# Optimization experiments

Measured on AMD Instinct MI355X. Metric: run time of the kernel, lower is better.

Reference implementation:

```python
import jax, jax.numpy as jnp
import numpy as np

DIM = 768
HEADS = 12
HID = 3072  # mlp_ratio * dim
BATCH = 8
FRAMES = 16
GRID = 14
NTOK = GRID * GRID
LN_EPS = 1e-5
EPS = 1e-6


def setup_inputs() -> dict:
    key = jax.random.key(0)
    ks = jax.random.split(key, 8)
    w = lambda k, shape: jax.random.normal(k, shape, jnp.float32) * 0.02
    return {
        "x": jax.random.normal(ks[0], (BATCH * FRAMES, NTOK, DIM), jnp.float32),
        "ln1_w": jnp.ones((DIM,), jnp.float32),
        "ln1_b": jnp.zeros((DIM,), jnp.float32),
        "qkv_w": w(ks[1], (3 * DIM, DIM)),
        "proj_w": w(ks[2], (DIM, DIM)),
        "proj_b": jnp.zeros((DIM,), jnp.float32),
        "ln2_w": jnp.ones((DIM,), jnp.float32),
        "ln2_b": jnp.zeros((DIM,), jnp.float32),
        "fc1_w": w(ks[3], (HID, DIM)),
        "fc1_b": jnp.zeros((HID,), jnp.float32),
        "dw_w": w(ks[4], (HID, 1, 3, 3)),
        "dw_b": jnp.zeros((HID,), jnp.float32),
        "fc2_w": w(ks[5], (DIM, HID)),
        "fc2_b": jnp.zeros((DIM,), jnp.float32),
        "H": GRID,
        "W": GRID,
        "num_frames": FRAMES,
    }


def _layernorm(x, w, b):
    mu = jnp.mean(x, axis=-1, keepdims=True)
    var = jnp.mean(jnp.square(x - mu), axis=-1, keepdims=True)
    return (x - mu) * jax.lax.rsqrt(var + LN_EPS) * w + b


def _joint_ts_attention(xn, qkv_w, proj_w, proj_b, num_frames):
    # xn: (b*f, n, c)
    Bt, n, C = xn.shape
    h = HEADS
    e = C // h
    scale = e ** (-0.5)
    qkv = jnp.einsum('bnc,dc->bnd', xn, qkv_w).reshape(Bt, n, 3, h, e)
    q, k, v = qkv[:, :, 0], qkv[:, :, 1], qkv[:, :, 2]
    # ReLU feature map + scale offset
    q_ = jax.nn.relu(q) + scale
    k_ = jax.nn.relu(k) + scale
    b = Bt // num_frames
    m = num_frames * n  # joint time-space sequence length
    q_ = q_.reshape(b, m, h, e)
    k_ = k_.reshape(b, m, h, e)
    v_ = v.reshape(b, m, h, e)
    # kv_: (b, h, e, e)
    kv = jnp.einsum('bnhe,bnhd->bhed', k_, v_)
    k_sum = jnp.sum(k_, axis=1)  # (b, h, e)
    z = 1.0 / (jnp.einsum('bnhe,bhe->bnh', q_, k_sum) + EPS)  # (b, m, h)
    out = jnp.einsum('bnhe,bhed->bnhd', q_, kv) * z[..., None]  # (b, m, h, e)
    out = out.reshape(Bt, n, C)
    return jnp.einsum('bnc,dc->bnd', out, proj_w) + proj_b


def _dwconv(x, w, b, H, W):
    # x: (B, N, C) -> NCHW depthwise 3x3, pad 1
    Bn, n, c = x.shape
    xi = jnp.transpose(x, (0, 2, 1)).reshape(Bn, c, H, W)
    y = jax.lax.conv_general_dilated(
        xi, w, window_strides=(1, 1), padding=((1, 1), (1, 1)),
        dimension_numbers=('NCHW', 'OIHW', 'NCHW'), feature_group_count=c)
    y = y + b[None, :, None, None]
    return jnp.transpose(y.reshape(Bn, c, n), (0, 2, 1))


def reference(x, ln1_w, ln1_b, qkv_w, proj_w, proj_b, ln2_w, ln2_b,
              fc1_w, fc1_b, dw_w, dw_b, fc2_w, fc2_b, H, W, num_frames):
    # x = x + attn(norm1(x), num_frames)
    x = x + _joint_ts_attention(_layernorm(x, ln1_w, ln1_b), qkv_w, proj_w, proj_b, num_frames)
    # x = x + mlp(norm2(x), H, W)
    xn = _layernorm(x, ln2_w, ln2_b)
    hdn = jnp.einsum('bnc,hc->bnh', xn, fc1_w) + fc1_b
    hdn = _dwconv(hdn, dw_w, dw_b, H, W)
    hdn = jax.nn.gelu(hdn, approximate=False)
    out = jnp.einsum('bnh,ch->bnc', hdn, fc2_w) + fc2_b
    return x + out
```

## Files before the change

kernel.cpp:

```cpp
#include <hip/hip_runtime.h>

typedef unsigned short u16;
typedef unsigned int u32;

typedef __bf16 bf16x8 __attribute__((ext_vector_type(8)));
typedef float f32x4 __attribute__((ext_vector_type(4)));

#define DIM 768
#define HID 3072
#define NTOK 196
#define BT 128
#define NTOKENS (BT * NTOK)
#define MJ 3136
#define HEADS 12

#define QB_ELE ((size_t)NTOKENS * 768)

#define SZ_WB   ((size_t)(2304*768 + 768*768 + 3072*768 + 768*3072) * 2)
#define SZ_XN   ((size_t)NTOKENS * DIM * 2)
#define SZ_QKV  ((size_t)NTOKENS * 2304 * 2)
#define SZ_X2   ((size_t)NTOKENS * DIM * 4)
#define SZ_HDN  ((size_t)NTOKENS * HID * 2)
#define SZ_KV   ((size_t)96 * 4096 * 4)
#define SZ_KS   ((size_t)96 * 64 * 4)
#define WS_NEED (SZ_WB + SZ_XN + SZ_QKV + SZ_X2 + SZ_HDN + SZ_KV + SZ_KS)

static void* g_buf = nullptr;

__device__ __forceinline__ float b2f(u16 u) {
  union { u32 i; float f; } x; x.i = ((u32)u) << 16; return x.f;
}
__device__ __forceinline__ u16 f2b(float f) {
  u32 x = __float_as_uint(f);
  return (u16)((x + 0x7fffu + ((x >> 16) & 1u)) >> 16);
}

__device__ __forceinline__ void gload_lds16(const u16* g, u16* l) {
  __builtin_amdgcn_global_load_lds(
      (const __attribute__((address_space(1))) u32*)g,
      (__attribute__((address_space(3))) u32*)l, 16, 0, 0);
}

#define N4_QKV   442368
#define N4_PROJ  147456
#define N4_FC1   589824
#define N4_FC2   589824
#define N4_ALL   (N4_QKV + N4_PROJ + N4_FC1 + N4_FC2)
__global__ __launch_bounds__(256) void cvt_all(const float* __restrict__ a,
    const float* __restrict__ b, const float* __restrict__ c,
    const float* __restrict__ d, u16* __restrict__ out)
{
  int i = blockIdx.x * 256 + threadIdx.x;
  if (i >= N4_ALL) return;
  const float* src;
  int j = i;
  if (j < N4_QKV) { src = a; }
  else if ((j -= N4_QKV) < N4_PROJ) { src = b; }
  else if ((j -= N4_PROJ) < N4_FC1) { src = c; }
  else { j -= N4_FC1; src = d; }
  float4 f = ((const float4*)src)[j];
  ushort4 r;
  r.x = f2b(f.x); r.y = f2b(f.y); r.z = f2b(f.z); r.w = f2b(f.w);
  ((ushort4*)out)[i] = r;
}

__global__ __launch_bounds__(256) void zero_f32(float* __restrict__ p, int n) {
  int i = blockIdx.x * 256 + threadIdx.x;
  if (i < n) p[i] = 0.0f;
}

__global__ __launch_bounds__(256) void ln_kernel(const float* __restrict__ xin,
    const float* __restrict__ w, const float* __restrict__ b, u16* __restrict__ out)
{
  const int token = blockIdx.x * 4 + (threadIdx.x >> 6);
  const int lane = threadIdx.x & 63;
  float v[12];
  const float* x = xin + (size_t)token * DIM;
#pragma unroll
  for (int c = 0; c < 3; ++c) {
    float4 f = *(const float4*)(x + c * 256 + lane * 4);
    v[c*4+0] = f.x; v[c*4+1] = f.y; v[c*4+2] = f.z; v[c*4+3] = f.w;
  }
  float s = 0.f, sq = 0.f;
#pragma unroll
  for (int i = 0; i < 12; ++i) { s += v[i]; sq += v[i] * v[i]; }
#pragma unroll
  for (int off = 32; off > 0; off >>= 1) {
    s += __shfl_xor(s, off, 64);
    sq += __shfl_xor(sq, off, 64);
  }
  const float mean = s * (1.0f / 768.0f);
  const float var = sq * (1.0f / 768.0f) - mean * mean;
  const float rstd = rsqrtf(var + 1e-5f);
  u16* o = out + (size_t)token * DIM;
#pragma unroll
  for (int c = 0; c < 3; ++c) {
    float4 wv = *(const float4*)(w + c * 256 + lane * 4);
    float4 bv = *(const float4*)(b + c * 256 + lane * 4);
    ushort4 r;
    r.x = f2b((v[c*4+0] - mean) * rstd * wv.x + bv.x);
    r.y = f2b((v[c*4+1] - mean) * rstd * wv.y + bv.y);
    r.z = f2b((v[c*4+2] - mean) * rstd * wv.z + bv.z);
    r.w = f2b((v[c*4+3] - mean) * rstd * wv.w + bv.w);
    *(ushort4*)(o + c * 256 + lane * 4) = r;
  }
}

template<int MODE, int NF, int NXT, int NN, int KK>
__global__ __launch_bounds__(512, 2) void gemm8(
    const u16* __restrict__ A, const u16* __restrict__ W,
    const float* __restrict__ bias, const float* __restrict__ res,
    void* __restrict__ out)
{
  extern __shared__ char smem[];
  u16* As = (u16*)smem;
  u16* Bs = (u16*)(smem + 65536);

  const int t = threadIdx.x;
  const int l = t & 63;
  const int w = t >> 6;
  const int wm = w >> 2;
  const int wn = w & 3;
  constexpr int NR = NF - 2;

  constexpr int TOTAL = 98 * NXT;
  constexpr int Q8 = TOTAL >> 3;
  constexpr int R8 = TOTAL & 7;
  const int orig = blockIdx.x;
  const int xcd = orig & 7;
  const int idx = orig >> 3;
  const int wg = (xcd < R8) ? (xcd * (Q8 + 1) + idx)
                            : (R8 * (Q8 + 1) + (xcd - R8) * Q8 + idx);
  const int m0 = (wg / NXT) * 256;
  const int n0 = (wg % NXT) * (NF * 64);

  const int scol = ((l & 7) ^ (l >> 3)) * 8;
  const u16* gA = A + (size_t)(m0 + w * 8 + (l >> 3)) * KK + scol;
  const u16* gB = W + (size_t)(n0 + w * 8 + (l >> 3)) * KK + scol;
  u16* lA = As + w * 512;
  u16* lB = Bs + w * 512;

#define STAGE_A(bb, u, kt) \
    gload_lds16(gA + (size_t)(u) * 64 * KK + (size_t)(kt) * 64, \
                lA + (bb) * 16384 + (u) * 4096)
#define STAGE_B(bb, u, kt) \
    gload_lds16(gB + (size_t)(u) * 64 * KK + (size_t)(kt) * 64, \
                lB + (bb) * NF * 4096 + (u) * 4096)

  const int lm = l & 15;
  const int qq = l >> 4;
  const int acol = (qq << 4) ^ ((l & 7) << 4);
  const int abase = (wm * 128 + lm) * 128 + acol;
  const int bbase = (wn * (NF * 16) + lm) * 128 + acol;

  f32x4 acc[8][NF];
#pragma unroll
  for (int mi = 0; mi < 8; ++mi)
#pragma unroll
    for (int ni = 0; ni < NF; ++ni) acc[mi][ni] = (f32x4){0.f, 0.f, 0.f, 0.f};

  constexpr int NT = KK / 64;

#pragma unroll
  for (int u = 0; u < 4; ++u) STAGE_A(0, u, 0);
#pragma unroll
  for (int u = 0; u < NF; ++u) STAGE_B(0, u, 0);
#pragma unroll
  for (int u = 0; u < 4; ++u) STAGE_A(1, u, 1);
  asm volatile("s_waitcnt vmcnt(4)" ::: "memory");
  __builtin_amdgcn_s_barrier();

  for (int ti = 0; ti < NT; ++ti) {
    const int cb = ti & 1, nb = cb ^ 1;
    const char* Ac = (const char*)As + cb * 32768;
    const char* Bc = (const char*)Bs + cb * (NF * 8192);
    bf16x8 a0[4][2], a1[4][2], b01[2][2], bx[NR][2];

#pragma unroll
    for (int mi = 0; mi < 4; ++mi) {
      const int off = abase + mi * 2048;
      a0[mi][0] = *(const bf16x8*)(Ac + off);
      a0[mi][1] = *(const bf16x8*)(Ac + (off ^ 64));
    }
#pragma unroll
    for (int ni = 0; ni < 2; ++ni) {
      const int off = bbase + ni * 2048;
      b01[ni][0] = *(const bf16x8*)(Bc + off);
      b01[ni][1] = *(const bf16x8*)(Bc + (off ^ 64));
    }
    if (ti + 1 < NT) { STAGE_B(nb, 0, ti + 1); STAGE_B(nb, 1, ti + 1); }
    __builtin_amdgcn_s_setprio(1);
#pragma unroll
    for (int mi = 0; mi < 4; ++mi)
#pragma unroll
      for (int ni = 0; ni < 2; ++ni) {
        acc[mi][ni] = __builtin_amdgcn_mfma_f32_16x16x32_bf16(a0[mi][0], b01[ni][0], acc[mi][ni], 0, 0, 0);
        acc[mi][ni] = __builtin_amdgcn_mfma_f32_16x16x32_bf16(a0[mi][1], b01[ni][1], acc[mi][ni], 0, 0, 0);
      }
    __builtin_amdgcn_s_setprio(0);

#pragma unroll
    for (int ni = 0; ni < NR; ++ni) {
      const int off = bbase + (ni + 2) * 2048;
      bx[ni][0] = *(const bf16x8*)(Bc + off);
      bx[ni][1] = *(const bf16x8*)(Bc + (off ^ 64));
    }
    if (ti + 1 < NT) {
#pragma unroll
      for (int u = 2; u < NF; ++u) STAGE_B(nb, u, ti + 1);
    }
    __builtin_amdgcn_s_setprio(1);
#pragma unroll
    for (int mi = 0; mi < 4; ++mi)
#pragma unroll
      for (int ni = 0; ni < NR; ++ni) {
        acc[mi][ni + 2] = __builtin_amdgcn_mfma_f32_16x16x32_bf16(a0[mi][0], bx[ni][0], acc[mi][ni + 2], 0, 0, 0);
        acc[mi][ni + 2] = __builtin_amdgcn_mfma_f32_16x16x32_bf16(a0[mi][1], bx[ni][1], acc[mi][ni + 2], 0, 0, 0);
      }
    __builtin_amdgcn_s_setprio(0);

#pragma unroll
    for (int mi = 0; mi < 4; ++mi) {
      const int off = abase + 8192 + mi * 2048;
      a1[mi][0] = *(const bf16x8*)(Ac + off);
      a1[mi][1] = *(const bf16x8*)(Ac + (off ^ 64));
    }
    __builtin_amdgcn_s_setprio(1);
#pragma unroll
    for (int mi = 0; mi < 4; ++mi)
#pragma unroll
      for (int ni = 0; ni < NR; ++ni) {
        acc[mi + 4][ni + 2] = __builtin_amdgcn_mfma_f32_16x16x32_bf16(a1[mi][0], bx[ni][0], acc[mi + 4][ni + 2], 0, 0, 0);
        acc[mi + 4][ni + 2] = __builtin_amdgcn_mfma_f32_16x16x32_bf16(a1[mi][1], bx[ni][1], acc[mi + 4][ni + 2], 0, 0, 0);
      }
    __builtin_amdgcn_s_setprio(0);

    asm volatile("s_waitcnt lgkmcnt(0)" ::: "memory");
    __builtin_amdgcn_s_barrier();

    if (ti + 2 < NT) {
#pragma unroll
      for (int u = 0; u < 4; ++u) STAGE_A(cb, u, ti + 2);
    }

    __builtin_amdgcn_s_setprio(1);
#pragma unroll
    for (int mi = 0; mi < 4; ++mi)
#pragma unroll
      for (int ni = 0; ni < 2; ++ni) {
        acc[mi + 4][ni] = __builtin_amdgcn_mfma_f32_16x16x32_bf16(a1[mi][0], b01[ni][0], acc[mi + 4][ni], 0, 0, 0);
        acc[mi + 4][ni] = __builtin_amdgcn_mfma_f32_16x16x32_bf16(a1[mi][1], b01[ni][1], acc[mi + 4][ni], 0, 0, 0);
      }
    __builtin_amdgcn_s_setprio(0);

    if (ti + 2 < NT) {
      asm volatile("s_waitcnt vmcnt(4)" ::: "memory");
    } else {
      asm volatile("s_waitcnt vmcnt(0)" ::: "memory");
    }
    __builtin_amdgcn_s_barrier();
  }
#undef STAGE_A
#undef STAGE_B

#pragma unroll
  for (int mi = 0; mi < 8; ++mi) {
    const int rbase = m0 + wm * 128 + mi * 16 + qq * 4;
    const int b = rbase / 3136;
    const int mj = rbase - b * 3136;
#pragma unroll
    for (int ni = 0; ni < NF; ++ni) {
      const int col = n0 + wn * (NF * 16) + ni * 16 + lm;
      if (MODE == 0) {
        if (col < 768) {
#pragma unroll
          for (int r = 0; r < 4; ++r) {
            float v = fmaxf(acc[mi][ni][r], 0.0f) + 0.125f;
            ((u16*)out)[(size_t)(rbase + r) * 768 + col] = f2b(v);
          }
        } else {
          const bool isV = (col >= 1536);
          const int cc = col - (isV ? 1536 : 768);
          const int h = cc >> 6, e = cc & 63;
          ushort4 pk;
          float v0 = acc[mi][ni][0], v1 = acc[mi][ni][1];
          float v2 = acc[mi][ni][2], v3 = acc[mi][ni][3];
          if (!isV) {
            v0 = fmaxf(v0, 0.0f) + 0.125f; v1 = fmaxf(v1, 0.0f) + 0.125f;
            v2 = fmaxf(v2, 0.0f) + 0.125f; v3 = fmaxf(v3, 0.0f) + 0.125f;
          }
          pk.x = f2b(v0); pk.y = f2b(v1); pk.z = f2b(v2); pk.w = f2b(v3);
          u16* dst = (u16*)out + (isV ? 2 * QB_ELE : QB_ELE)
                   + ((size_t)((b * 12 + h) * 64 + e)) * 3136 + mj;
          *(ushort4*)dst = pk;
        }
      } else {
        const float bv = bias[col];
#pragma unroll
        for (int r = 0; r < 4; ++r) {
          float v = acc[mi][ni][r];
          const size_t idxo = (size_t)(rbase + r) * NN + col;
          if (MODE == 1) {
            ((float*)out)[idxo] = v + bv + res[idxo];
          } else if (MODE == 2) {
            ((u16*)out)[idxo] = f2b(v + bv);
          } else {
            ((float*)out)[idxo] = v + bv + res[idxo];
          }
        }
      }
    }
  }
}

__global__ __launch_bounds__(256) void ksum_kernel(const u16* __restrict__ KT,
    float* __restrict__ KS)
{
  const int bh = blockIdx.x;
  const int t = threadIdx.x;
  const int w = t >> 6, l = t & 63;
  const u16* base = KT + (size_t)(bh * 64 + w * 16) * 3136;
  for (int r = 0; r < 16; ++r) {
    float s = 0.f;
    const u16* row = base + (size_t)r * 3136;
#pragma unroll
    for (int p = 0; p < 7; ++p) {
      const int m = p * 512 + l * 8;
      if (m < 3136) {
        bf16x8 v = *(const bf16x8*)(row + m);
#pragma unroll
        for (int j = 0; j < 8; ++j) s += (float)v[j];
      }
    }
#pragma unroll
    for (int off = 32; off > 0; off >>= 1) s += __shfl_xor(s, off, 64);
    if (l == 0) KS[bh * 64 + w * 16 + r] = s;
  }
}

__global__ __launch_bounds__(256) void kv_mfma(const u16* __restrict__ KT,
    const u16* __restrict__ VT, float* __restrict__ kv)
{
  const int bh = blockIdx.x;
  const int s = blockIdx.y;
  const int t = threadIdx.x;
  const int l = t & 63, w = t >> 6;
  const int lm = l & 15, qq = l >> 4;
  const size_t mj0 = (size_t)s * 448;
  const u16* ka = KT + (size_t)(bh * 64 + w * 16 + lm) * 3136 + mj0 + qq * 8;
  const u16* vb = VT + (size_t)(bh * 64 + lm) * 3136 + mj0 + qq * 8;

  f32x4 acc[4];
#pragma unroll
  for (int ni = 0; ni < 4; ++ni) acc[ni] = (f32x4){0.f, 0.f, 0.f, 0.f};

#pragma unroll 4
  for (int kk = 0; kk < 14; ++kk) {
    bf16x8 a = *(const bf16x8*)(ka + kk * 32);
#pragma unroll
    for (int ni = 0; ni < 4; ++ni) {
      bf16x8 b = *(const bf16x8*)(vb + (size_t)ni * 16 * 3136 + kk * 32);
      acc[ni] = __builtin_amdgcn_mfma_f32_16x16x32_bf16(a, b, acc[ni], 0, 0, 0);
    }
  }
  float* dst = kv + (size_t)bh * 4096;
#pragma unroll
  for (int ni = 0; ni < 4; ++ni)
#pragma unroll
    for (int r = 0; r < 4; ++r)
      atomicAdd(&dst[(w * 16 + qq * 4 + r) * 64 + ni * 16 + lm], acc[ni][r]);
}

__global__ __launch_bounds__(256) void attn_out(const u16* __restrict__ qb,
    const float* __restrict__ kv, const float* __restrict__ ksum,
    u16* __restrict__ outp)
{
  const int chunk = blockIdx.x;
  const int h = blockIdx.y;
  const int b = blockIdx.z;
  __shared__ float kvs[4096];
  __shared__ float kss[64];
  __shared__ float qs[4096];
  const int t = threadIdx.x;
  const float* kvsrc = kv + (size_t)(b * 12 + h) * 4096;
  for (int i = t; i < 1024; i += 256)
    ((float4*)kvs)[i] = ((const float4*)kvsrc)[i];
  if (t < 64) kss[t] = ksum[(b * 12 + h) * 64 + t];
  __syncthreads();
  const int wv = t >> 6, lane = t & 63;
  float* qw = &qs[wv * 1024];
  const size_t tok0 = (size_t)b * MJ + chunk * 64 + wv * 16;
#pragma unroll
  for (int i = 0; i < 16; ++i) {
    float q = b2f(qb[(tok0 + i) * 768 + h * 64 + lane]);
    float pd = q * kss[lane];
#pragma unroll
    for (int off = 32; off > 0; off >>= 1) pd += __shfl_xor(pd, off, 64);
    qw[i * 64 + lane] = q * (1.0f / (pd + 1e-6f));
  }
  float o[16];
#pragma unroll
  for (int i = 0; i < 16; ++i) o[i] = 0.f;
  for (int e = 0; e < 64; ++e) {
    const float kvc = kvs[e * 64 + lane];
#pragma unroll
    for (int i = 0; i < 16; ++i) o[i] += qw[i * 64 + e] * kvc;
  }
#pragma unroll
  for (int i = 0; i < 16; ++i)
    outp[(tok0 + i) * 768 + h * 64 + lane] = f2b(o[i]);
}

__global__ __launch_bounds__(256) void dwconv_gelu(u16* __restrict__ hdn,
    const float* __restrict__ w, const float* __restrict__ bias)
{
  __shared__ u16 pl[196 * 136];
  const int cb = blockIdx.x;
  const int fr = blockIdx.y;
  const int t = threadIdx.x;
  const int c0 = cb * 128;
  u16* base = hdn + (size_t)fr * 196 * HID + c0;
#pragma unroll
  for (int i = 0; i < 13; ++i) {
    int idx = i * 256 + t;
    if (idx < 3136) {
      int p = idx >> 4, cq = idx & 15;
      *(uint4*)&pl[p * 136 + cq * 8] = *(const uint4*)(base + (size_t)p * HID + cq * 8);
    }
  }
  __syncthreads();
  const int pc = t & 31;
  const int pg = t >> 5;
  const int cc = pc * 4;
  float wr[36];
#pragma unroll
  for (int k = 0; k < 9; ++k)
#pragma unroll
    for (int u = 0; u < 4; ++u) wr[k * 4 + u] = w[(c0 + cc + u) * 9 + k];
  float bv[4];
#pragma unroll
  for (int u = 0; u < 4; ++u) bv[u] = bias[c0 + cc + u];

  for (int j = 0; j < 25; ++j) {
    const int p = pg + j * 8;
    if (p >= 196) break;
    const int py = p / 14, px = p % 14;
    float a0 = bv[0], a1 = bv[1], a2 = bv[2], a3 = bv[3];
#pragma unroll
    for (int ky = 0; ky < 3; ++ky) {
      int yy = py + ky - 1;
      if (yy < 0 || yy > 13) continue;
#pragma unroll
      for (int kx = 0; kx < 3; ++kx) {
        int xx = px + kx - 1;
        if (xx < 0 || xx > 13) continue;
        ushort4 tv = *(const ushort4*)&pl[(yy * 14 + xx) * 136 + cc];
        const float* wk = &wr[(ky * 3 + kx) * 4];
        a0 += wk[0] * b2f(tv.x);
        a1 += wk[1] * b2f(tv.y);
        a2 += wk[2] * b2f(tv.z);
        a3 += wk[3] * b2f(tv.w);
      }
    }
    ushort4 r;
    r.x = f2b(0.5f * a0 * (1.0f + erff(a0 * 0.70710678118654752f)));
    r.y = f2b(0.5f * a1 * (1.0f + erff(a1 * 0.70710678118654752f)));
    r.z = f2b(0.5f * a2 * (1.0f + erff(a2 * 0.70710678118654752f)));
    r.w = f2b(0.5f * a3 * (1.0f + erff(a3 * 0.70710678118654752f)));
    *(ushort4*)(base + (size_t)p * HID + cc) = r;
  }
}

static void set_gemm_attrs() {
  (void)hipFuncSetAttribute(reinterpret_cast<const void*>(&gemm8<0, 4, 9, 2304, 768>),
                            hipFuncAttributeMaxDynamicSharedMemorySize, 131072);
  (void)hipFuncSetAttribute(reinterpret_cast<const void*>(&gemm8<1, 3, 4, 768, 768>),
                            hipFuncAttributeMaxDynamicSharedMemorySize, 114688);
  (void)hipFuncSetAttribute(reinterpret_cast<const void*>(&gemm8<2, 4, 12, 3072, 768>),
                            hipFuncAttributeMaxDynamicSharedMemorySize, 131072);
  (void)hipFuncSetAttribute(reinterpret_cast<const void*>(&gemm8<3, 3, 4, 768, 3072>),
                            hipFuncAttributeMaxDynamicSharedMemorySize, 114688);
}
struct WsInit {
  WsInit() {
    (void)hipMalloc(&g_buf, WS_NEED);
    set_gemm_attrs();
  }
};
static WsInit g_wsinit;

extern "C" void kernel_launch(void* const* d_in, const int* in_sizes, int n_in,
                              void* d_out, int out_size, void* d_ws, size_t ws_size,
                              hipStream_t stream)
{
  (void)in_sizes; (void)n_in; (void)out_size;
  static bool attrs_once = [] { set_gemm_attrs(); return true; }();
  (void)attrs_once;

  const float* x     = (const float*)d_in[0];
  const float* ln1w  = (const float*)d_in[1];
  const float* ln1b  = (const float*)d_in[2];
  const float* qkvw  = (const float*)d_in[3];
  const float* projw = (const float*)d_in[4];
  const float* projb = (const float*)d_in[5];
  const float* ln2w  = (const float*)d_in[6];
  const float* ln2b  = (const float*)d_in[7];
  const float* fc1w  = (const float*)d_in[8];
  const float* fc1b  = (const float*)d_in[9];
  const float* dww   = (const float*)d_in[10];
  const float* dwb   = (const float*)d_in[11];
  const float* fc2w  = (const float*)d_in[12];
  const float* fc2b  = (const float*)d_in[13];

  char* p = (ws_size >= WS_NEED) ? (char*)d_ws : (char*)g_buf;
  u16* WQKV  = (u16*)p;   p += (size_t)2304 * 768 * 2;
  u16* WPROJ = (u16*)p;   p += (size_t)768 * 768 * 2;
  u16* WFC1  = (u16*)p;   p += (size_t)3072 * 768 * 2;
  u16* WFC2  = (u16*)p;   p += (size_t)768 * 3072 * 2;
  u16* XN    = (u16*)p;   p += SZ_XN;
  u16* QKV   = (u16*)p;   p += SZ_QKV;
  float* X2  = (float*)p; p += SZ_X2;
  u16* HDN   = (u16*)p;   p += SZ_HDN;
  float* KV  = (float*)p; p += SZ_KV;
  float* KS  = (float*)p; p += SZ_KS;

  u16* KT = QKV + QB_ELE;
  u16* VT = QKV + 2 * QB_ELE;

  cvt_all<<<(N4_ALL + 255) / 256, 256, 0, stream>>>(qkvw, projw, fc1w, fc2w, WQKV);

  const int nz = 96 * 4096;
  zero_f32<<<(nz + 255) / 256, 256, 0, stream>>>(KV, nz);
  ln_kernel<<<NTOKENS / 4, 256, 0, stream>>>(x, ln1w, ln1b, XN);
  gemm8<0, 4, 9, 2304, 768><<<98 * 9, 512, 131072, stream>>>(XN, WQKV, nullptr, nullptr, QKV);
  ksum_kernel<<<96, 256, 0, stream>>>(KT, KS);
  kv_mfma<<<dim3(96, 7), 256, 0, stream>>>(KT, VT, KV);
  attn_out<<<dim3(49, 12, 8), 256, 0, stream>>>(QKV, KV, KS, XN);
  gemm8<1, 3, 4, 768, 768><<<98 * 4, 512, 114688, stream>>>(XN, WPROJ, projb, x, X2);
  ln_kernel<<<NTOKENS / 4, 256, 0, stream>>>(X2, ln2w, ln2b, QKV);
  gemm8<2, 4, 12, 3072, 768><<<98 * 12, 512, 131072, stream>>>(QKV, WFC1, fc1b, nullptr, HDN);
  dwconv_gelu<<<dim3(24, 128), 256, 0, stream>>>(HDN, dww, dwb);
  gemm8<3, 3, 4, 768, 3072><<<98 * 4, 512, 114688, stream>>>(HDN, WFC2, fc2b, X2, (float*)d_out);
}
```

Baseline: 909.5 us.

## Shrink GEMM tiles to 128 rows with 4 waves and single-buffered static LDS

The GEMM kernel moves from 256-row tiles with 8 waves and double-buffered dynamic LDS (up to 128KB) to 128-row tiles with 4 waves and a single static LDS buffer. Each k-step now waits for all loads, reads fragments, barriers, then issues the next tile's global loads before running the MFMAs. The grid doubles, which should raise occupancy and smooth wave quantization across CUs. In exchange, per-tile reuse drops, the hand-interleaved load/MFMA schedule is gone, and global-to-LDS latency is hidden only by other resident workgroups.

```diff
diff --git a/kernel.cpp b/kernel.cpp
--- a/kernel.cpp
+++ b/kernel.cpp
@@ -107,23 +107,21 @@
 }
 
 template<int MODE, int NF, int NXT, int NN, int KK>
-__global__ __launch_bounds__(512, 2) void gemm8(
+__global__ __launch_bounds__(256, 2) void gemm8(
     const u16* __restrict__ A, const u16* __restrict__ W,
     const float* __restrict__ bias, const float* __restrict__ res,
     void* __restrict__ out)
 {
-  extern __shared__ char smem[];
-  u16* As = (u16*)smem;
-  u16* Bs = (u16*)(smem + 65536);
+  __shared__ __align__(16) u16 As[128 * 64];
+  __shared__ __align__(16) u16 Bs[NF * 64 * 64];
 
   const int t = threadIdx.x;
   const int l = t & 63;
   const int w = t >> 6;
-  const int wm = w >> 2;
-  const int wn = w & 3;
-  constexpr int NR = NF - 2;
-
-  constexpr int TOTAL = 98 * NXT;
+  const int wmh = w >> 1;
+  const int wnh = w & 1;
+
+  constexpr int TOTAL = 196 * NXT;
   constexpr int Q8 = TOTAL >> 3;
   constexpr int R8 = TOTAL & 7;
   const int orig = blockIdx.x;
@@ -131,151 +129,95 @@
   const int idx = orig >> 3;
   const int wg = (xcd < R8) ? (xcd * (Q8 + 1) + idx)
                             : (R8 * (Q8 + 1) + (xcd - R8) * Q8 + idx);
-  const int m0 = (wg / NXT) * 256;
+  const int m0 = (wg / NXT) * 128;
   const int n0 = (wg % NXT) * (NF * 64);
 
   const int scol = ((l & 7) ^ (l >> 3)) * 8;
-  const u16* gA = A + (size_t)(m0 + w * 8 + (l >> 3)) * KK + scol;
-  const u16* gB = W + (size_t)(n0 + w * 8 + (l >> 3)) * KK + scol;
-  u16* lA = As + w * 512;
-  u16* lB = Bs + w * 512;
-
-#define STAGE_A(bb, u, kt) \
+  const u16* gA = A + (size_t)(m0 + w * 16 + (l >> 3)) * KK + scol;
+  const u16* gB = W + (size_t)(n0 + w * 16 + (l >> 3)) * KK + scol;
+  u16* lA = As + w * 1024;
+  u16* lB = Bs + w * 1024;
+
+#define STAGE_A(u, kt) do { \
     gload_lds16(gA + (size_t)(u) * 64 * KK + (size_t)(kt) * 64, \
-                lA + (bb) * 16384 + (u) * 4096)
-#define STAGE_B(bb, u, kt) \
+                lA + (u) * 4096); \
+    gload_lds16(gA + (size_t)(u) * 64 * KK + (size_t)8 * KK + (size_t)(kt) * 64, \
+                lA + (u) * 4096 + 512); } while (0)
+#define STAGE_B(u, kt) do { \
     gload_lds16(gB + (size_t)(u) * 64 * KK + (size_t)(kt) * 64, \
-                lB + (bb) * NF * 4096 + (u) * 4096)
+                lB + (u) * 4096); \
+    gload_lds16(gB + (size_t)(u) * 64 * KK + (size_t)8 * KK + (size_t)(kt) * 64, \
+                lB + (u) * 4096 + 512); } while (0)
+#define STAGE_ALL(kt) do { \
+    STAGE_A(0, kt); STAGE_A(1, kt); \
+    _Pragma("unroll") \
+    for (int u_ = 0; u_ < NF; ++u_) STAGE_B(u_, kt); } while (0)
 
   const int lm = l & 15;
   const int qq = l >> 4;
   const int acol = (qq << 4) ^ ((l & 7) << 4);
-  const int abase = (wm * 128 + lm) * 128 + acol;
-  const int bbase = (wn * (NF * 16) + lm) * 128 + acol;
-
-  f32x4 acc[8][NF];
-#pragma unroll
-  for (int mi = 0; mi < 8; ++mi)
-#pragma unroll
-    for (int ni = 0; ni < NF; ++ni) acc[mi][ni] = (f32x4){0.f, 0.f, 0.f, 0.f};
+  const int abase = (wmh * 64 + lm) * 128 + acol;
+  const int bbase = (wnh * (NF * 32) + lm) * 128 + acol;
+
+  f32x4 acc[4][2 * NF];
+#pragma unroll
+  for (int mi = 0; mi < 4; ++mi)
+#pragma unroll
+    for (int nj = 0; nj < 2 * NF; ++nj) acc[mi][nj] = (f32x4){0.f, 0.f, 0.f, 0.f};
 
   constexpr int NT = KK / 64;
 
-#pragma unroll
-  for (int u = 0; u < 4; ++u) STAGE_A(0, u, 0);
-#pragma unroll
-  for (int u = 0; u < NF; ++u) STAGE_B(0, u, 0);
-#pragma unroll
-  for (int u = 0; u < 4; ++u) STAGE_A(1, u, 1);
-  asm volatile("s_waitcnt vmcnt(4)" ::: "memory");
-  __builtin_amdgcn_s_barrier();
+  STAGE_ALL(0);
 
   for (int ti = 0; ti < NT; ++ti) {
-    const int cb = ti & 1, nb = cb ^ 1;
-    const char* Ac = (const char*)As + cb * 32768;
-    const char* Bc = (const char*)Bs + cb * (NF * 8192);
-    bf16x8 a0[4][2], a1[4][2], b01[2][2], bx[NR][2];
-
+    asm volatile("s_waitcnt vmcnt(0)" ::: "memory");
+    __builtin_amdgcn_s_barrier();
+
+    bf16x8 af[4][2], bfv[2 * NF][2];
 #pragma unroll
     for (int mi = 0; mi < 4; ++mi) {
       const int off = abase + mi * 2048;
-      a0[mi][0] = *(const bf16x8*)(Ac + off);
-      a0[mi][1] = *(const bf16x8*)(Ac + (off ^ 64));
-    }
-#pragma unroll
-    for (int ni = 0; ni < 2; ++ni) {
-      const int off = bbase + ni * 2048;
-      b01[ni][0] = *(const bf16x8*)(Bc + off);
-      b01[ni][1] = *(const bf16x8*)(Bc + (off ^ 64));
-    }
-    if (ti + 1 < NT) { STAGE_B(nb, 0, ti + 1); STAGE_B(nb, 1, ti + 1); }
+      af[mi][0] = *(const bf16x8*)((const char*)As + off);
+      af[mi][1] = *(const bf16x8*)((const char*)As + (off ^ 64));
+    }
+#pragma unroll
+    for (int nj = 0; nj < 2 * NF; ++nj) {
+      const int off = bbase + nj * 2048;
+      bfv[nj][0] = *(const bf16x8*)((const char*)Bs + off);
+      bfv[nj][1] = *(const bf16x8*)((const char*)Bs + (off ^ 64));
+    }
+    asm volatile("s_waitcnt lgkmcnt(0)" ::: "memory");
+    __builtin_amdgcn_s_barrier();
+
+    if (ti + 1 < NT) STAGE_ALL(ti + 1);
+
     __builtin_amdgcn_s_setprio(1);
 #pragma unroll
     for (int mi = 0; mi < 4; ++mi)
 #pragma unroll
-      for (int ni = 0; ni < 2; ++ni) {
-        acc[mi][ni] = __builtin_amdgcn_mfma_f32_16x16x32_bf16(a0[mi][0], b01[ni][0], acc[mi][ni], 0, 0, 0);
-        acc[mi][ni] = __builtin_amdgcn_mfma_f32_16x16x32_bf16(a0[mi][1], b01[ni][1], acc[mi][ni], 0, 0, 0);
+      for (int nj = 0; nj < 2 * NF; ++nj) {
+        acc[mi][nj] = __builtin_amdgcn_mfma_f32_16x16x32_bf16(af[mi][0], bfv[nj][0], acc[mi][nj], 0, 0, 0);
+        acc[mi][nj] = __builtin_amdgcn_mfma_f32_16x16x32_bf16(af[mi][1], bfv[nj][1], acc[mi][nj], 0, 0, 0);
       }
     __builtin_amdgcn_s_setprio(0);
-
-#pragma unroll
-    for (int ni = 0; ni < NR; ++ni) {
-      const int off = bbase + (ni + 2) * 2048;
-      bx[ni][0] = *(const bf16x8*)(Bc + off);
-      bx[ni][1] = *(const bf16x8*)(Bc + (off ^ 64));
-    }
-    if (ti + 1 < NT) {
-#pragma unroll
-      for (int u = 2; u < NF; ++u) STAGE_B(nb, u, ti + 1);
-    }
-    __builtin_amdgcn_s_setprio(1);
-#pragma unroll
-    for (int mi = 0; mi < 4; ++mi)
-#pragma unroll
-      for (int ni = 0; ni < NR; ++ni) {
-        acc[mi][ni + 2] = __builtin_amdgcn_mfma_f32_16x16x32_bf16(a0[mi][0], bx[ni][0], acc[mi][ni + 2], 0, 0, 0);
-        acc[mi][ni + 2] = __builtin_amdgcn_mfma_f32_16x16x32_bf16(a0[mi][1], bx[ni][1], acc[mi][ni + 2], 0, 0, 0);
-      }
-    __builtin_amdgcn_s_setprio(0);
-
-#pragma unroll
-    for (int mi = 0; mi < 4; ++mi) {
-      const int off = abase + 8192 + mi * 2048;
-      a1[mi][0] = *(const bf16x8*)(Ac + off);
-      a1[mi][1] = *(const bf16x8*)(Ac + (off ^ 64));
-    }
-    __builtin_amdgcn_s_setprio(1);
-#pragma unroll
-    for (int mi = 0; mi < 4; ++mi)
-#pragma unroll
-      for (int ni = 0; ni < NR; ++ni) {
-        acc[mi + 4][ni + 2] = __builtin_amdgcn_mfma_f32_16x16x32_bf16(a1[mi][0], bx[ni][0], acc[mi + 4][ni + 2], 0, 0, 0);
-        acc[mi + 4][ni + 2] = __builtin_amdgcn_mfma_f32_16x16x32_bf16(a1[mi][1], bx[ni][1], acc[mi + 4][ni + 2], 0, 0, 0);
-      }
-    __builtin_amdgcn_s_setprio(0);
-
-    asm volatile("s_waitcnt lgkmcnt(0)" ::: "memory");
-    __builtin_amdgcn_s_barrier();
-
-    if (ti + 2 < NT) {
-#pragma unroll
-      for (int u = 0; u < 4; ++u) STAGE_A(cb, u, ti + 2);
-    }
-
-    __builtin_amdgcn_s_setprio(1);
-#pragma unroll
-    for (int mi = 0; mi < 4; ++mi)
-#pragma unroll
-      for (int ni = 0; ni < 2; ++ni) {
-        acc[mi + 4][ni] = __builtin_amdgcn_mfma_f32_16x16x32_bf16(a1[mi][0], b01[ni][0], acc[mi + 4][ni], 0, 0, 0);
-        acc[mi + 4][ni] = __builtin_amdgcn_mfma_f32_16x16x32_bf16(a1[mi][1], b01[ni][1], acc[mi + 4][ni], 0, 0, 0);
-      }
-    __builtin_amdgcn_s_setprio(0);
-
-    if (ti + 2 < NT) {
-      asm volatile("s_waitcnt vmcnt(4)" ::: "memory");
-    } else {
-      asm volatile("s_waitcnt vmcnt(0)" ::: "memory");
-    }
-    __builtin_amdgcn_s_barrier();
   }
 #undef STAGE_A
 #undef STAGE_B
-
-#pragma unroll
-  for (int mi = 0; mi < 8; ++mi) {
-    const int rbase = m0 + wm * 128 + mi * 16 + qq * 4;
+#undef STAGE_ALL
+
+#pragma unroll
+  for (int mi = 0; mi < 4; ++mi) {
+    const int rbase = m0 + wmh * 64 + mi * 16 + qq * 4;
     const int b = rbase / 3136;
     const int mj = rbase - b * 3136;
 #pragma unroll
-    for (int ni = 0; ni < NF; ++ni) {
-      const int col = n0 + wn * (NF * 16) + ni * 16 + lm;
+    for (int nj = 0; nj < 2 * NF; ++nj) {
+      const int col = n0 + wnh * (NF * 32) + nj * 16 + lm;
       if (MODE == 0) {
         if (col < 768) {
 #pragma unroll
           for (int r = 0; r < 4; ++r) {
-            float v = fmaxf(acc[mi][ni][r], 0.0f) + 0.125f;
+            float v = fmaxf(acc[mi][nj][r], 0.0f) + 0.125f;
             ((u16*)out)[(size_t)(rbase + r) * 768 + col] = f2b(v);
           }
         } else {
@@ -283,8 +225,8 @@
           const int cc = col - (isV ? 1536 : 768);
           const int h = cc >> 6, e = cc & 63;
           ushort4 pk;
-          float v0 = acc[mi][ni][0], v1 = acc[mi][ni][1];
-          float v2 = acc[mi][ni][2], v3 = acc[mi][ni][3];
+          float v0 = acc[mi][nj][0], v1 = acc[mi][nj][1];
+          float v2 = acc[mi][nj][2], v3 = acc[mi][nj][3];
           if (!isV) {
             v0 = fmaxf(v0, 0.0f) + 0.125f; v1 = fmaxf(v1, 0.0f) + 0.125f;
             v2 = fmaxf(v2, 0.0f) + 0.125f; v3 = fmaxf(v3, 0.0f) + 0.125f;
@@ -298,7 +240,7 @@
         const float bv = bias[col];
 #pragma unroll
         for (int r = 0; r < 4; ++r) {
-          float v = acc[mi][ni][r];
+          float v = acc[mi][nj][r];
           const size_t idxo = (size_t)(rbase + r) * NN + col;
           if (MODE == 1) {
             ((float*)out)[idxo] = v + bv + res[idxo];
@@ -471,21 +413,8 @@
   }
 }
 
-static void set_gemm_attrs() {
-  (void)hipFuncSetAttribute(reinterpret_cast<const void*>(&gemm8<0, 4, 9, 2304, 768>),
-                            hipFuncAttributeMaxDynamicSharedMemorySize, 131072);
-  (void)hipFuncSetAttribute(reinterpret_cast<const void*>(&gemm8<1, 3, 4, 768, 768>),
-                            hipFuncAttributeMaxDynamicSharedMemorySize, 114688);
-  (void)hipFuncSetAttribute(reinterpret_cast<const void*>(&gemm8<2, 4, 12, 3072, 768>),
-                            hipFuncAttributeMaxDynamicSharedMemorySize, 131072);
-  (void)hipFuncSetAttribute(reinterpret_cast<const void*>(&gemm8<3, 3, 4, 768, 3072>),
-                            hipFuncAttributeMaxDynamicSharedMemorySize, 114688);
-}
 struct WsInit {
-  WsInit() {
-    (void)hipMalloc(&g_buf, WS_NEED);
-    set_gemm_attrs();
-  }
+  WsInit() { (void)hipMalloc(&g_buf, WS_NEED); }
 };
 static WsInit g_wsinit;
 
@@ -494,8 +423,6 @@
                               hipStream_t stream)
 {
   (void)in_sizes; (void)n_in; (void)out_size;
-  static bool attrs_once = [] { set_gemm_attrs(); return true; }();
-  (void)attrs_once;
 
   const float* x     = (const float*)d_in[0];
   const float* ln1w  = (const float*)d_in[1];
@@ -532,13 +459,13 @@
   const int nz = 96 * 4096;
   zero_f32<<<(nz + 255) / 256, 256, 0, stream>>>(KV, nz);
   ln_kernel<<<NTOKENS / 4, 256, 0, stream>>>(x, ln1w, ln1b, XN);
-  gemm8<0, 4, 9, 2304, 768><<<98 * 9, 512, 131072, stream>>>(XN, WQKV, nullptr, nullptr, QKV);
+  gemm8<0, 4, 9, 2304, 768><<<196 * 9, 256, 0, stream>>>(XN, WQKV, nullptr, nullptr, QKV);
   ksum_kernel<<<96, 256, 0, stream>>>(KT, KS);
   kv_mfma<<<dim3(96, 7), 256, 0, stream>>>(KT, VT, KV);
   attn_out<<<dim3(49, 12, 8), 256, 0, stream>>>(QKV, KV, KS, XN);
-  gemm8<1, 3, 4, 768, 768><<<98 * 4, 512, 114688, stream>>>(XN, WPROJ, projb, x, X2);
+  gemm8<1, 3, 4, 768, 768><<<196 * 4, 256, 0, stream>>>(XN, WPROJ, projb, x, X2);
   ln_kernel<<<NTOKENS / 4, 256, 0, stream>>>(X2, ln2w, ln2b, QKV);
-  gemm8<2, 4, 12, 3072, 768><<<98 * 12, 512, 131072, stream>>>(QKV, WFC1, fc1b, nullptr, HDN);
+  gemm8<2, 4, 12, 3072, 768><<<196 * 12, 256, 0, stream>>>(QKV, WFC1, fc1b, nullptr, HDN);
   dwconv_gelu<<<dim3(24, 128), 256, 0, stream>>>(HDN, dww, dwb);
-  gemm8<3, 3, 4, 768, 3072><<<98 * 4, 512, 114688, stream>>>(HDN, WFC2, fc2b, X2, (float*)d_out);
-}
+  gemm8<3, 3, 4, 768, 3072><<<196 * 4, 256, 0, stream>>>(HDN, WFC2, fc2b, X2, (float*)d_out);
+}
```

Result: no change. 896.6 us (-1.4%).
